# Kernel tuning notes

Measured on AMD Instinct MI355X. Metric: run time of the kernel, lower is better.

## Reference

```python
import jax, jax.numpy as jnp
import numpy as np

N_QUBITS = 6
N_LAYERS = 2
QSVT_DEGREE = 3
BATCH = 128
SEQ_LEN = 512
DIM = 2 ** N_QUBITS
# wire 0 is the most-significant bit in the statevector index (PennyLane convention)
_POP = np.array([bin(i).count('1') for i in range(DIM)], dtype=np.float32)
PHASE_SIGN = jnp.asarray(N_QUBITS - 2.0 * _POP)  # (DIM,): sum_w (1 - 2*bit_w)


def _rx(t):
    c = jnp.cos(0.5 * t).astype(jnp.complex64)
    s = (-1j * jnp.sin(0.5 * t)).astype(jnp.complex64)
    return jnp.stack([jnp.stack([c, s]), jnp.stack([s, c])])


def _ry(t):
    c = jnp.cos(0.5 * t).astype(jnp.complex64)
    s = jnp.sin(0.5 * t).astype(jnp.complex64)
    return jnp.stack([jnp.stack([c, -s]), jnp.stack([s, c])])


def _rz(t):
    e = jnp.exp(-0.5j * t.astype(jnp.complex64))
    z = jnp.zeros((), jnp.complex64)
    return jnp.stack([jnp.stack([e, z]), jnp.stack([z, jnp.conj(e)])])


def _apply_1q(psi, U, w):
    # psi: (B,) + (2,)*N_QUBITS ; U: (2,2) complex, same for all batch elems
    psi = jnp.moveaxis(psi, 1 + w, -1)
    psi = psi @ U.T
    return jnp.moveaxis(psi, -1, 1 + w)


def _apply_ry_batched(psi, theta, w):
    # RY with a per-batch angle theta: (B,)
    psi = jnp.moveaxis(psi, 1 + w, -1)
    c = jnp.cos(0.5 * theta).reshape((-1,) + (1,) * (N_QUBITS - 1))
    s = jnp.sin(0.5 * theta).reshape((-1,) + (1,) * (N_QUBITS - 1))
    a, b = psi[..., 0], psi[..., 1]
    psi = jnp.stack([c * a - s * b, s * a + c * b], axis=-1)
    return jnp.moveaxis(psi, -1, 1 + w)


def _cnot(psi, c, t):
    p0 = jax.lax.index_in_dim(psi, 0, axis=1 + c, keepdims=True)
    p1 = jax.lax.index_in_dim(psi, 1, axis=1 + c, keepdims=True)
    p1 = jnp.flip(p1, axis=1 + t)
    return jnp.concatenate([p0, p1], axis=1 + c)


def _circuit_step(h, x, params, poly):
    # h, x: (B, N_QUBITS) angles. Returns <Z_w> per qubit: (B, N_QUBITS).
    B = h.shape[0]
    # 1) state encoding: RY(h_w)|0> = cos(h/2)|0> + sin(h/2)|1>  (product state)
    c, s = jnp.cos(0.5 * h), jnp.sin(0.5 * h)
    psi = jnp.ones((B, 1), jnp.complex64)
    for w in range(N_QUBITS):
        amp = jnp.stack([c[:, w], s[:, w]], axis=-1).astype(jnp.complex64)  # (B,2)
        psi = (psi[:, :, None] * amp[:, None, :]).reshape(B, -1)
    psi = psi.reshape((B,) + (2,) * N_QUBITS)
    # 2) QSVT block: RZ(coeff*pi) on every wire fuses into one diagonal phase
    for d in range(QSVT_DEGREE + 1):
        theta = poly[d] * np.pi
        phase = jnp.exp((-0.5j) * theta * PHASE_SIGN)  # (DIM,)
        psi = (psi.reshape(B, -1) * phase[None, :]).reshape((B,) + (2,) * N_QUBITS)
        for i in range(N_QUBITS - 1):
            psi = _cnot(psi, i, i + 1)
        psi = _cnot(psi, N_QUBITS - 1, 0)  # ring closure
    # 3) variational layers: per-wire RZ@RY@RX (RX applied first), then CNOT chain
    idx = 0
    for _ in range(N_LAYERS):
        for i in range(N_QUBITS):
            U = _rz(params[idx + 2]) @ _ry(params[idx + 1]) @ _rx(params[idx])
            psi = _apply_1q(psi, U, i)
            idx += 3
        for i in range(N_QUBITS - 1):
            psi = _cnot(psi, i, i + 1)
    # 4) input injection: RY(x_w) with per-batch angles
    for w in range(N_QUBITS):
        psi = _apply_ry_batched(psi, x[:, w], w)
    # 5) measurement: <Z_w> = P(bit_w=0) - P(bit_w=1)
    p = jnp.abs(psi) ** 2
    zs = []
    for w in range(N_QUBITS):
        axes = tuple(a for a in range(1, N_QUBITS + 1) if a != 1 + w)
        pw = p.sum(axis=axes)  # (B,2)
        zs.append(pw[:, 0] - pw[:, 1])
    return jnp.stack(zs, axis=-1)


def _ssm_pass(angles, params, poly, reverse):
    a = jnp.flip(angles, axis=1) if reverse else angles
    xs = jnp.moveaxis(a, 1, 0)  # (T, B, n)
    h0 = jnp.zeros((a.shape[0], N_QUBITS), jnp.float32)

    def step(h, x):
        hn = _circuit_step(h, x, params, poly)
        return hn, hn

    _, ys = jax.lax.scan(step, h0, xs)
    out = jnp.moveaxis(ys, 0, 1)  # (B, T, n)
    return jnp.flip(out, axis=1) if reverse else out


def setup_inputs() -> dict:
    key = jax.random.key(0)
    k0, k1, k2, k3 = jax.random.split(key, 4)
    angles = jax.random.uniform(k0, (BATCH, SEQ_LEN, N_QUBITS), jnp.float32) * np.float32(np.pi)
    poly_coeffs = jax.random.normal(k1, (QSVT_DEGREE + 1,), jnp.float32) * 0.1
    fwd_params = jax.random.normal(k2, (N_QUBITS * N_LAYERS * 3,), jnp.float32) * 0.1
    bwd_params = jax.random.normal(k3, (N_QUBITS * N_LAYERS * 3,), jnp.float32) * 0.1
    fwd_coeff = jnp.full((1,), 0.5, jnp.float32)
    bwd_coeff = jnp.full((1,), 0.5, jnp.float32)
    return {'angles': angles, 'poly_coeffs': poly_coeffs, 'fwd_params': fwd_params,
            'bwd_params': bwd_params, 'fwd_coeff': fwd_coeff, 'bwd_coeff': bwd_coeff}


def reference(angles, poly_coeffs, fwd_params, bwd_params, fwd_coeff, bwd_coeff):
    h_fwd = _ssm_pass(angles, fwd_params, poly_coeffs, reverse=False)
    h_bwd = _ssm_pass(angles, bwd_params, poly_coeffs, reverse=True)
    return jax.nn.sigmoid(fwd_coeff) * h_fwd + jax.nn.sigmoid(bwd_coeff) * h_bwd
```

## Files before the change

### kernel.cpp

```cpp
#include <hip/hip_runtime.h>
#include <hip/hip_bf16.h>
#include <stdint.h>

#define BATCH 128
#define SEQ   512
#define NW    6
#define DIM   64
#define NELEM (BATCH * SEQ * NW)
#define PI_F  3.14159265358979323846f

typedef float v2f __attribute__((ext_vector_type(2)));
typedef uint16_t u16x8 __attribute__((ext_vector_type(8)));

__device__ __forceinline__ v2f pkfma(float s, v2f m, v2f a) {
    return __builtin_elementwise_fma((v2f){s, s}, m, a);
}

template <int CTRL>
__device__ __forceinline__ void red_stage6(float v[6]) {
#pragma unroll
    for (int k = 0; k < 6; ++k)
        v[k] += __int_as_float(__builtin_amdgcn_update_dpp(
            0, __float_as_int(v[k]), CTRL, 0xF, 0xF, false));
}

__device__ __forceinline__ void sincos_half(float h, float& s, float& c) {
    const float u = h * h;
    c = fmaf(u, fmaf(u, 2.6041667e-3f, -0.125f), 1.0f);
    s = h * fmaf(u, fmaf(u, 2.6041667e-4f, -2.0833333e-2f), 0.5f);
}

__device__ __forceinline__ float ldf(const void* p, int i, bool bf) {
    if (bf) {
        uint32_t u = (uint32_t)((const uint16_t*)p)[i];
        return __uint_as_float(u << 16);
    }
    return ((const float*)p)[i];
}

__global__ void k_prep(const void* ang, const void* poly, const void* fp,
                       const void* bp, const void* fc, const void* bc,
                       float* __restrict__ misc, float* __restrict__ Mg,
                       int* __restrict__ flag) {
    __shared__ int cnt;
    if (threadIdx.x == 0) cnt = 0;
    __syncthreads();
    {
        uint32_t w = ((const uint32_t*)ang)[threadIdx.x & 255];
        uint32_t e = (w >> 8) & 0xFFu;
        if (e >= 0x3Au && e <= 0x41u) atomicAdd(&cnt, 1);
    }
    __syncthreads();
    const bool bf = (cnt >= 128);

    if (blockIdx.x == 32) {
        if (threadIdx.x == 0)      misc[76] = ldf(fc, 0, bf);
        else if (threadIdx.x == 1) misc[77] = ldf(bc, 0, bf);
        else if (threadIdx.x == 2) *flag = bf ? 1 : 0;
        return;
    }

    const int lane = threadIdx.x & 63;
    const int tix  = blockIdx.x * 4 + (threadIdx.x >> 6);
    const int dir  = tix >> 6;
    const int col  = tix & 63;
    const void* prm = dir ? bp : fp;
    const int p = lane;

    float yr = (p == col) ? 1.f : 0.f;
    float yi = 0.f;

#pragma unroll
    for (int d = 0; d < 4; ++d) {
        const float th = 0.5f * PI_F * ldf(poly, d, bf) *
                         (float)(6 - 2 * (int)__popc((unsigned)p));
        float s, c;
        __sincosf(th, &s, &c);
        const float nr = yr * c + yi * s;
        const float ni = yi * c - yr * s;
        yr = nr; yi = ni;
#pragma unroll
        for (int k = 0; k < 6; ++k) {
            const int cw = k, tw = (k + 1) % 6;
            const int src = p ^ (((p >> (5 - cw)) & 1) << (5 - tw));
            yr = __shfl(yr, src, 64);
            yi = __shfl(yi, src, 64);
        }
    }

    int idx = 0;
#pragma unroll
    for (int l = 0; l < 2; ++l) {
#pragma unroll
        for (int w = 0; w < 6; ++w) {
            float cx, sx, cy, sy, cz, sz;
            __sincosf(0.5f * ldf(prm, idx + 0, bf), &sx, &cx);
            __sincosf(0.5f * ldf(prm, idx + 1, bf), &sy, &cy);
            __sincosf(0.5f * ldf(prm, idx + 2, bf), &sz, &cz);
            idx += 3;
            const float A = cy * cx, B = sy * sx, C = sy * cx, D = cy * sx;
            const float U00r = cz * A + sz * B, U00i = cz * B - sz * A;
            const float U11r = U00r,            U11i = sz * A - cz * B;
            const float Xr   = cz * C + sz * D, Xi   = sz * C - cz * D;
            const int m  = 1 << (5 - w);
            const int bb = (p >> (5 - w)) & 1;
            const float C1r = bb ? U11r : U00r;
            const float C1i = bb ? U11i : U00i;
            const float C2r = bb ? Xr : -Xr;
            const float C2i = Xi;
            const float pr = __shfl_xor(yr, m, 64);
            const float pi = __shfl_xor(yi, m, 64);
            const float nr = C1r * yr - C1i * yi + C2r * pr - C2i * pi;
            const float ni = C1r * yi + C1i * yr + C2r * pi + C2i * pr;
            yr = nr; yi = ni;
        }
#pragma unroll
        for (int k = 0; k < 5; ++k) {
            const int src = p ^ (((p >> (5 - k)) & 1) << (5 - (k + 1)));
            yr = __shfl(yr, src, 64);
            yi = __shfl(yi, src, 64);
        }
    }

    float* out = Mg + ((size_t)(dir * 64 + p) * 64 + (size_t)col) * 2;
    out[0] = yr;
    out[1] = yi;
}

__global__ void __launch_bounds__(64, 1) k_sim(const void* __restrict__ ang,
                                               const float* __restrict__ Mg,
                                               float* __restrict__ hbuf,
                                               const int* __restrict__ flag) {
    const int lane  = threadIdx.x;
    const int chain = blockIdx.x;
    const int dir   = chain >> 7;
    const int b     = chain & 127;
    const bool bf   = (*flag != 0);

    __shared__ __align__(16) float cl[SEQ * 12];
    __shared__ __align__(16) float zb[SEQ * NW];

    if (!bf) {
        const float4* src =
            (const float4*)((const float*)ang + (size_t)b * (SEQ * NW));
#pragma unroll
        for (int k = 0; k < 12; ++k) {
            const int v = k * 64 + lane;
            const float4 a = src[v];
            __align__(16) float o[8];
            float s, c;
            __sincosf(a.x, &s, &c); o[0] = c; o[1] = s;
            __sincosf(a.y, &s, &c); o[2] = c; o[3] = s;
            __sincosf(a.z, &s, &c); o[4] = c; o[5] = s;
            __sincosf(a.w, &s, &c); o[6] = c; o[7] = s;
            ((float4*)cl)[2 * v]     = ((const float4*)o)[0];
            ((float4*)cl)[2 * v + 1] = ((const float4*)o)[1];
        }
    } else {
        const u16x8* src =
            (const u16x8*)((const uint16_t*)ang + (size_t)b * (SEQ * NW));
#pragma unroll
        for (int k = 0; k < 6; ++k) {
            const int v = k * 64 + lane;
            const u16x8 a = src[v];
            __align__(16) float o[16];
#pragma unroll
            for (int e = 0; e < 8; ++e) {
                const float x = __uint_as_float(((uint32_t)a[e]) << 16);
                float s, c;
                __sincosf(x, &s, &c);
                o[2 * e] = c; o[2 * e + 1] = s;
            }
#pragma unroll
            for (int j = 0; j < 4; ++j)
                ((float4*)cl)[4 * v + j] = ((const float4*)o)[j];
        }
    }

    v2f Mc[64];
    {
        const float4* mr4 =
            (const float4*)(Mg + (size_t)(dir * 64 + lane) * 128);
#pragma unroll
        for (int k = 0; k < 32; ++k) {
            const float4 m = mr4[k];
            Mc[2 * k]     = (v2f){m.x, m.y};
            Mc[2 * k + 1] = (v2f){m.z, m.w};
        }
    }

    int zmask[6];
#pragma unroll
    for (int w = 0; w < 6; ++w) zmask[w] = ((lane >> (5 - w)) & 1) << 31;
    const int bpa0 = (lane ^ 32) << 2;

    const float* cp = cl + (dir ? (SEQ - 1) * 12 : 0);
    const int   cstep = dir ? -12 : 12;
    float*       zp = zb + (dir ? (SEQ - 1) * NW : 0);
    const int   zstep = dir ? -NW : NW;

    float h[6] = {0.f, 0.f, 0.f, 0.f, 0.f, 0.f};

    __syncthreads();

    for (int t = 0; t < SEQ; ++t) {
        const float4 xq0 = ((const float4*)cp)[0];
        const float4 xq1 = ((const float4*)cp)[1];
        const float4 xq2 = ((const float4*)cp)[2];
        cp += cstep;

        float cw[6], sw[6];
#pragma unroll
        for (int w = 0; w < 6; ++w) sincos_half(h[w], sw[w], cw[w]);
        float g01[4], g45[4], eH[8], eL[8];
        g01[0] = cw[0] * cw[1]; g01[1] = cw[0] * sw[1];
        g01[2] = sw[0] * cw[1]; g01[3] = sw[0] * sw[1];
        g45[0] = cw[4] * cw[5]; g45[1] = cw[4] * sw[5];
        g45[2] = sw[4] * cw[5]; g45[3] = sw[4] * sw[5];
#pragma unroll
        for (int j = 0; j < 8; ++j) {
            eH[j] = g01[j >> 1] * ((j & 1) ? sw[2] : cw[2]);
            eL[j] = ((j >> 2) ? sw[3] : cw[3]) * g45[j & 3];
        }

        v2f y = {0.f, 0.f};
#pragma unroll
        for (int jh = 0; jh < 8; ++jh) {
            v2f n = {0.f, 0.f};
#pragma unroll
            for (int jl = 0; jl < 8; ++jl)
                n = pkfma(eL[jl], Mc[8 * jh + jl], n);
            y = pkfma(eH[jh], n, y);
        }
        const float yr = y.x, yi = y.y;
        const int yri = __float_as_int(yr), yii = __float_as_int(yi);

        float pr[6], pi[6];
        pr[0] = __int_as_float(__builtin_amdgcn_ds_bpermute(bpa0, yri));
        pi[0] = __int_as_float(__builtin_amdgcn_ds_bpermute(bpa0, yii));
        pr[1] = __int_as_float(__builtin_amdgcn_ds_swizzle(yri, 0x401F));
        pi[1] = __int_as_float(__builtin_amdgcn_ds_swizzle(yii, 0x401F));
        pr[2] = __int_as_float(__builtin_amdgcn_ds_swizzle(yri, 0x201F));
        pi[2] = __int_as_float(__builtin_amdgcn_ds_swizzle(yii, 0x201F));
        pr[3] = __int_as_float(__builtin_amdgcn_ds_swizzle(yri, 0x101F));
        pi[3] = __int_as_float(__builtin_amdgcn_ds_swizzle(yii, 0x101F));
        pr[4] = __int_as_float(__builtin_amdgcn_update_dpp(0, yri, 0x4E, 0xF, 0xF, false));
        pi[4] = __int_as_float(__builtin_amdgcn_update_dpp(0, yii, 0x4E, 0xF, 0xF, false));
        pr[5] = __int_as_float(__builtin_amdgcn_update_dpp(0, yri, 0xB1, 0xF, 0xF, false));
        pi[5] = __int_as_float(__builtin_amdgcn_update_dpp(0, yii, 0xB1, 0xF, 0xF, false));

        const float q = fmaf(yr, yr, yi * yi);
        const float cx[6] = {xq0.x, xq0.z, xq1.x, xq1.z, xq2.x, xq2.z};
        const float sx[6] = {xq0.y, xq0.w, xq1.y, xq1.w, xq2.y, xq2.w};

        float v[6];
#pragma unroll
        for (int w = 0; w < 6; ++w) {
            const float cq  = __int_as_float(__float_as_int(cx[w] * q) ^ zmask[w]);
            const float dot = fmaf(yr, pr[w], yi * pi[w]);
            v[w] = fmaf(-sx[w], dot, cq);
        }

        red_stage6<0x111>(v);
        red_stage6<0x112>(v);
        red_stage6<0x114>(v);
        red_stage6<0x118>(v);
        red_stage6<0x142>(v);
        red_stage6<0x143>(v);

        if (lane == 63) {
#pragma unroll
            for (int w = 0; w < 6; ++w) zp[w] = v[w];
        }
        zp += zstep;
#pragma unroll
        for (int w = 0; w < 6; ++w)
            h[w] = __int_as_float(
                __builtin_amdgcn_readlane(__float_as_int(v[w]), 63));
    }

    __syncthreads();

    {
        float* orow = hbuf + (size_t)dir * NELEM + (size_t)b * (SEQ * NW);
        const float4* zs4 = (const float4*)zb;
        float4* go = (float4*)orow;
#pragma unroll
        for (int k = 0; k < 12; ++k) {
            const int idx = k * 64 + lane;
            go[idx] = zs4[idx];
        }
    }
}

__global__ void k_combine(const float* __restrict__ hbuf,
                          const float* __restrict__ misc,
                          void* __restrict__ out, const int* __restrict__ flag) {
    const int i = blockIdx.x * blockDim.x + threadIdx.x;
    if (i >= NELEM) return;
    const float sf = 1.f / (1.f + __expf(-misc[76]));
    const float sb = 1.f / (1.f + __expf(-misc[77]));
    const float v = sf * hbuf[i] + sb * hbuf[NELEM + i];
    if (*flag) ((__hip_bfloat16*)out)[i] = __float2bfloat16(v);
    else       ((float*)out)[i] = v;
}

extern "C" void kernel_launch(void* const* d_in, const int* in_sizes, int n_in,
                              void* d_out, int out_size, void* d_ws, size_t ws_size,
                              hipStream_t stream) {
    const void* ang  = d_in[0];
    const void* poly = d_in[1];
    const void* fp   = d_in[2];
    const void* bp   = d_in[3];
    const void* fc   = d_in[4];
    const void* bc   = d_in[5];

    float* misc = (float*)d_ws + 32;
    float* hbuf = misc + 128;
    float* Mg   = hbuf + 2 * NELEM;
    int*   flag = (int*)(Mg + 2 * 64 * 64 * 2);

    k_prep<<<33, 256, 0, stream>>>(ang, poly, fp, bp, fc, bc, misc, Mg, flag);
    k_sim<<<256, 64, 0, stream>>>(ang, Mg, hbuf, flag);
    k_combine<<<(NELEM + 255) / 256, 256, 0, stream>>>(hbuf, misc, d_out, flag);
}
```

Measured before the change: 379.5 us.

## Split matrix between registers and LDS, use permlane swaps for lane exchange

Half of each lane's 64 complex matrix coefficients now stays in registers. The other half is stored in a transposed LDS layout that k_prep writes and that is reloaded as float4 every timestep, which lowers register pressure in the serial recurrence. The lane-partner exchanges that used ds_bpermute and ds_swizzle are replaced by permlane32/16 swaps and a DPP row rotate, avoiding LDS round trips. The trade is 16 LDS float4 reads per step inside the latency-bound loop, in exchange for fewer registers and cheaper cross-lane shuffles.

```diff
diff --git a/kernel.cpp b/kernel.cpp
--- a/kernel.cpp
+++ b/kernel.cpp
@@ -24,6 +24,12 @@
             0, __float_as_int(v[k]), CTRL, 0xF, 0xF, false));
 }
 
+template <int CTRL>
+__device__ __forceinline__ float dpp_mov(float x) {
+    return __int_as_float(__builtin_amdgcn_update_dpp(
+        0, __float_as_int(x), CTRL, 0xF, 0xF, false));
+}
+
 __device__ __forceinline__ void sincos_half(float h, float& s, float& c) {
     const float u = h * h;
     c = fmaf(u, fmaf(u, 2.6041667e-3f, -0.125f), 1.0f);
@@ -41,7 +47,7 @@
 __global__ void k_prep(const void* ang, const void* poly, const void* fp,
                        const void* bp, const void* fc, const void* bc,
                        float* __restrict__ misc, float* __restrict__ Mg,
-                       int* __restrict__ flag) {
+                       float* __restrict__ Mgt, int* __restrict__ flag) {
     __shared__ int cnt;
     if (threadIdx.x == 0) cnt = 0;
     __syncthreads();
@@ -125,10 +131,17 @@
     float* out = Mg + ((size_t)(dir * 64 + p) * 64 + (size_t)col) * 2;
     out[0] = yr;
     out[1] = yi;
+    if (col >= 32) {
+        const int pp = (col - 32) >> 1;
+        float2* mt = (float2*)(Mgt +
+            (((size_t)(dir * 16 + pp) * 64 + p) * 2 + (col & 1)) * 2);
+        *mt = (float2){yr, yi};
+    }
 }
 
 __global__ void __launch_bounds__(64, 1) k_sim(const void* __restrict__ ang,
                                                const float* __restrict__ Mg,
+                                               const float* __restrict__ Mgt,
                                                float* __restrict__ hbuf,
                                                const int* __restrict__ flag) {
     const int lane  = threadIdx.x;
@@ -137,8 +150,9 @@
     const int b     = chain & 127;
     const bool bf   = (*flag != 0);
 
-    __shared__ __align__(16) float cl[SEQ * 12];
-    __shared__ __align__(16) float zb[SEQ * NW];
+    __shared__ __align__(16) float  cl[SEQ * 12];
+    __shared__ __align__(16) float  zb[SEQ * NW];
+    __shared__ float4 mlds[16 * 64];
 
     if (!bf) {
         const float4* src =
@@ -177,22 +191,28 @@
         }
     }
 
-    v2f Mc[64];
+    {
+        const float4* mgt4 = (const float4*)Mgt;
+#pragma unroll
+        for (int k = 0; k < 16; ++k)
+            mlds[k * 64 + lane] = mgt4[(size_t)(dir * 16 + k) * 64 + lane];
+    }
+
+    v2f Mreg[32];
     {
         const float4* mr4 =
             (const float4*)(Mg + (size_t)(dir * 64 + lane) * 128);
 #pragma unroll
-        for (int k = 0; k < 32; ++k) {
+        for (int k = 0; k < 16; ++k) {
             const float4 m = mr4[k];
-            Mc[2 * k]     = (v2f){m.x, m.y};
-            Mc[2 * k + 1] = (v2f){m.z, m.w};
+            Mreg[2 * k]     = (v2f){m.x, m.y};
+            Mreg[2 * k + 1] = (v2f){m.z, m.w};
         }
     }
 
     int zmask[6];
 #pragma unroll
     for (int w = 0; w < 6; ++w) zmask[w] = ((lane >> (5 - w)) & 1) << 31;
-    const int bpa0 = (lane ^ 32) << 2;
 
     const float* cp = cl + (dir ? (SEQ - 1) * 12 : 0);
     const int   cstep = dir ? -12 : 12;
@@ -204,6 +224,9 @@
     __syncthreads();
 
     for (int t = 0; t < SEQ; ++t) {
+        float4 mb[16];
+#pragma unroll
+        for (int k = 0; k < 16; ++k) mb[k] = mlds[k * 64 + lane];
         const float4 xq0 = ((const float4*)cp)[0];
         const float4 xq1 = ((const float4*)cp)[1];
         const float4 xq2 = ((const float4*)cp)[2];
@@ -225,29 +248,48 @@
 
         v2f y = {0.f, 0.f};
 #pragma unroll
-        for (int jh = 0; jh < 8; ++jh) {
+        for (int jh = 0; jh < 4; ++jh) {
             v2f n = {0.f, 0.f};
 #pragma unroll
             for (int jl = 0; jl < 8; ++jl)
-                n = pkfma(eL[jl], Mc[8 * jh + jl], n);
+                n = pkfma(eL[jl], Mreg[8 * jh + jl], n);
             y = pkfma(eH[jh], n, y);
+        }
+#pragma unroll
+        for (int g = 0; g < 4; ++g) {
+            v2f n = {0.f, 0.f};
+#pragma unroll
+            for (int j2 = 0; j2 < 4; ++j2) {
+                const float4 Q = mb[4 * g + j2];
+                n = pkfma(eL[2 * j2],     (v2f){Q.x, Q.y}, n);
+                n = pkfma(eL[2 * j2 + 1], (v2f){Q.z, Q.w}, n);
+            }
+            y = pkfma(eH[4 + g], n, y);
         }
         const float yr = y.x, yi = y.y;
         const int yri = __float_as_int(yr), yii = __float_as_int(yi);
 
         float pr[6], pi[6];
-        pr[0] = __int_as_float(__builtin_amdgcn_ds_bpermute(bpa0, yri));
-        pi[0] = __int_as_float(__builtin_amdgcn_ds_bpermute(bpa0, yii));
-        pr[1] = __int_as_float(__builtin_amdgcn_ds_swizzle(yri, 0x401F));
-        pi[1] = __int_as_float(__builtin_amdgcn_ds_swizzle(yii, 0x401F));
-        pr[2] = __int_as_float(__builtin_amdgcn_ds_swizzle(yri, 0x201F));
-        pi[2] = __int_as_float(__builtin_amdgcn_ds_swizzle(yii, 0x201F));
         pr[3] = __int_as_float(__builtin_amdgcn_ds_swizzle(yri, 0x101F));
         pi[3] = __int_as_float(__builtin_amdgcn_ds_swizzle(yii, 0x101F));
-        pr[4] = __int_as_float(__builtin_amdgcn_update_dpp(0, yri, 0x4E, 0xF, 0xF, false));
-        pi[4] = __int_as_float(__builtin_amdgcn_update_dpp(0, yii, 0x4E, 0xF, 0xF, false));
-        pr[5] = __int_as_float(__builtin_amdgcn_update_dpp(0, yri, 0xB1, 0xF, 0xF, false));
-        pi[5] = __int_as_float(__builtin_amdgcn_update_dpp(0, yii, 0xB1, 0xF, 0xF, false));
+        {
+            auto r0 = __builtin_amdgcn_permlane32_swap(yri, yri, false, false);
+            auto r1 = __builtin_amdgcn_permlane32_swap(yii, yii, false, false);
+            pr[0] = __int_as_float((int)((lane & 32) ? r0[0] : r0[1]));
+            pi[0] = __int_as_float((int)((lane & 32) ? r1[0] : r1[1]));
+        }
+        {
+            auto r0 = __builtin_amdgcn_permlane16_swap(yri, yri, false, false);
+            auto r1 = __builtin_amdgcn_permlane16_swap(yii, yii, false, false);
+            pr[1] = __int_as_float((int)((lane & 16) ? r0[0] : r0[1]));
+            pi[1] = __int_as_float((int)((lane & 16) ? r1[0] : r1[1]));
+        }
+        pr[2] = dpp_mov<0x128>(yr);
+        pi[2] = dpp_mov<0x128>(yi);
+        pr[4] = dpp_mov<0x4E>(yr);
+        pi[4] = dpp_mov<0x4E>(yi);
+        pr[5] = dpp_mov<0xB1>(yr);
+        pi[5] = dpp_mov<0xB1>(yi);
 
         const float q = fmaf(yr, yr, yi * yi);
         const float cx[6] = {xq0.x, xq0.z, xq1.x, xq1.z, xq2.x, xq2.z};
@@ -318,9 +360,11 @@
     float* misc = (float*)d_ws + 32;
     float* hbuf = misc + 128;
     float* Mg   = hbuf + 2 * NELEM;
-    int*   flag = (int*)(Mg + 2 * 64 * 64 * 2);
-
-    k_prep<<<33, 256, 0, stream>>>(ang, poly, fp, bp, fc, bc, misc, Mg, flag);
-    k_sim<<<256, 64, 0, stream>>>(ang, Mg, hbuf, flag);
+    float* Mgt  = Mg + 2 * 64 * 64 * 2;
+    int*   flag = (int*)(Mgt + 2 * 16 * 64 * 4);
+
+    k_prep<<<33, 256, 0, stream>>>(ang, poly, fp, bp, fc, bc,
+                                   misc, Mg, Mgt, flag);
+    k_sim<<<256, 64, 0, stream>>>(ang, Mg, Mgt, hbuf, flag);
     k_combine<<<(NELEM + 255) / 256, 256, 0, stream>>>(hbuf, misc, d_out, flag);
 }
```

Measured after the change: 392.6 us. 1.03x slower.
